# Performance work log

Hardware: AMD Instinct MI355X
Metric: run time of the kernel (lower is better)

Reference implementation:

```python
import jax, jax.numpy as jnp
import numpy as np

N_FFT = 1024
N_STAGES = 4
BASE = N_FFT >> N_STAGES          # 64: base-case DFT size
N_CHUNKS = 1 << N_STAGES          # 16 chunks after permutation
SPLIT0 = N_FFT // 2 + 1           # rfft output length (513)


def _mod_seq(order):
    mset = [0]
    for o in range(order):
        step = 2 ** o
        mset = [v for x in mset for v in (x, x + step)]
    return mset


def _perm_matrix(N, order):
    # faithful replica of get_fft_permutation_matrix
    m = np.zeros((N, N), dtype=np.float32)
    base = 2 ** order
    k = 0
    for p in _mod_seq(order):
        for j in range(N // base):
            m[j * base + p, k] = 1.0
            k += 1
    return m


def _twiddle(n):
    w = np.exp(-2j * np.pi / n) ** np.arange(n // 2)
    return (jnp.asarray(w.real.astype(np.float32)),
            jnp.asarray(w.imag.astype(np.float32)))


PERM = jnp.asarray(_perm_matrix(N_FFT, N_STAGES))
_dft = np.fft.fft(np.eye(BASE))
DFT_R = jnp.asarray(_dft.real.astype(np.float32))
DFT_I = jnp.asarray(_dft.imag.astype(np.float32))
# twiddle stage s combines blocks of size (N_FFT >> (N_STAGES - s)) into twice that
TWIDDLES = [_twiddle(N_FFT >> (N_STAGES - 1 - s)) for s in range(N_STAGES)]


def setup_inputs() -> dict:
    key = jax.random.key(0)
    x = jax.random.normal(key, (16, 512, N_FFT), dtype=jnp.float32)
    return {"x": x}


def reference(x):
    # 1) bit-reversal-style permutation, expressed (faithfully) as a matmul
    y = jnp.matmul(x, PERM)                                   # [B,T,N]
    blocks = y.reshape(*x.shape[:-1], N_CHUNKS, BASE)         # [B,T,C,base]
    blocks = jnp.moveaxis(blocks, -2, 0)                      # [C,B,T,base]
    # 2) base-case DFT via dense matmul (all dfts share the same matrix)
    br = jnp.matmul(blocks, DFT_R.T)
    bi = jnp.matmul(blocks, DFT_I.T)
    # 3) Cooley-Tukey twiddle stages; consecutive blocks pair as (even, odd)
    for wr, wi in TWIDDLES:
        er, orr = br[0::2], br[1::2]
        ei, oii = bi[0::2], bi[1::2]
        tr = wr * orr - wi * oii
        ti = wr * oii + wi * orr
        br = jnp.concatenate([er + tr, er - tr], axis=-1)
        bi = jnp.concatenate([ei + ti, ei - ti], axis=-1)
    real, imag = br[0], bi[0]                                 # [B,T,N]
    # 4) keep only the rfft half-spectrum
    return real[..., :SPLIT0], imag[..., :SPLIT0]
```

## Files before the change

### kernel.cpp

```cpp
#include <hip/hip_runtime.h>

#define N_FFT 1024
#define SPLIT0 513
#define PAD(a) ((a) + ((a) >> 5))

__global__ __launch_bounds__(256) void rfft1024_pairs(const float* __restrict__ x,
                                                      float* __restrict__ out,
                                                      int nrows) {
    __shared__ float bre[2][N_FFT + 32];
    __shared__ float bim[2][N_FFT + 32];

    const int t = threadIdx.x;
    const int pair = blockIdx.x;
    const float* __restrict__ r0 = x + (size_t)(2 * pair) * N_FFT;
    const float* __restrict__ r1 = r0 + N_FFT;

    #pragma unroll
    for (int c = 0; c < 4; ++c) {
        int i = t + 256 * c;
        bre[0][PAD(i)] = r0[i];
        bim[0][PAD(i)] = r1[i];
    }
    __syncthreads();

    const float CANG = -6.2831853071795864769f / 1024.0f;
    int src = 0;

    #pragma unroll
    for (int p = 0; p < 5; ++p) {
        const int m = 1 << (2 * p);
        const int k = t & (m - 1);
        const int jm = t - k;

        float ar = bre[src][PAD(t)],       ai = bim[src][PAD(t)];
        float br = bre[src][PAD(t + 256)], bi = bim[src][PAD(t + 256)];
        float cr = bre[src][PAD(t + 512)], ci = bim[src][PAD(t + 512)];
        float dr = bre[src][PAD(t + 768)], di = bim[src][PAD(t + 768)];

        float t0r = ar + cr, t0i = ai + ci;
        float t1r = ar - cr, t1i = ai - ci;
        float t2r = br + dr, t2i = bi + di;
        float t3r = br - dr, t3i = bi - di;

        float y0r = t0r + t2r, y0i = t0i + t2i;
        float y1r = t1r + t3i, y1i = t1i - t3r;
        float y2r = t0r - t2r, y2i = t0i - t2i;
        float y3r = t1r - t3i, y3i = t1i + t3r;

        float ang = CANG * (float)jm;
        float s1, c1;
        __sincosf(ang, &s1, &c1);
        float c2 = c1 * c1 - s1 * s1, s2 = 2.0f * c1 * s1;
        float c3 = c1 * c2 - s1 * s2, s3 = c1 * s2 + s1 * c2;

        float z1r = y1r * c1 - y1i * s1, z1i = y1r * s1 + y1i * c1;
        float z2r = y2r * c2 - y2i * s2, z2i = y2r * s2 + y2i * c2;
        float z3r = y3r * c3 - y3i * s3, z3i = y3r * s3 + y3i * c3;

        const int dst = src ^ 1;
        const int w0 = k + 4 * jm;
        bre[dst][PAD(w0)]          = y0r; bim[dst][PAD(w0)]          = y0i;
        bre[dst][PAD(w0 + m)]      = z1r; bim[dst][PAD(w0 + m)]      = z1i;
        bre[dst][PAD(w0 + 2 * m)]  = z2r; bim[dst][PAD(w0 + 2 * m)]  = z2i;
        bre[dst][PAD(w0 + 3 * m)]  = z3r; bim[dst][PAD(w0 + 3 * m)]  = z3i;
        __syncthreads();
        src ^= 1;
    }

    const size_t row0 = (size_t)(2 * pair);
    float* __restrict__ outr = out;
    float* __restrict__ outi = out + (size_t)nrows * SPLIT0;

    #pragma unroll
    for (int c = 0; c < 2; ++c) {
        int kk = t + 256 * c;
        float zr = bre[src][PAD(kk)], zi = bim[src][PAD(kk)];
        int km = (N_FFT - kk) & (N_FFT - 1);
        float mr = bre[src][PAD(km)], mi = bim[src][PAD(km)];
        float X0r = 0.5f * (zr + mr), X0i = 0.5f * (zi - mi);
        float X1r = 0.5f * (zi + mi), X1i = 0.5f * (mr - zr);
        outr[row0 * SPLIT0 + kk]       = X0r;
        outi[row0 * SPLIT0 + kk]       = X0i;
        outr[(row0 + 1) * SPLIT0 + kk] = X1r;
        outi[(row0 + 1) * SPLIT0 + kk] = X1i;
    }
    if (t == 0) {
        float zr = bre[src][PAD(512)], zi = bim[src][PAD(512)];
        outr[row0 * SPLIT0 + 512]       = zr;
        outi[row0 * SPLIT0 + 512]       = 0.0f;
        outr[(row0 + 1) * SPLIT0 + 512] = zi;
        outi[(row0 + 1) * SPLIT0 + 512] = 0.0f;
    }
}

extern "C" void kernel_launch(void* const* d_in, const int* in_sizes, int n_in,
                              void* d_out, int out_size, void* d_ws, size_t ws_size,
                              hipStream_t stream) {
    const float* x = (const float*)d_in[0];
    float* out = (float*)d_out;
    const int nrows = in_sizes[0] / N_FFT;
    rfft1024_pairs<<<nrows / 2, 256, 0, stream>>>(x, out, nrows);
}
```

Measured before the change: 83.11 us.

## Restructure FFT as single-wave radix-16 register passes with fewer LDS exchanges

Replaces the 256-thread kernel, which ran five radix-4 passes each with a shared-memory round trip, with one 64-lane wavefront per row pair. Each lane now holds 16 complex points in registers and does two radix-4 stages (a radix-16 step) per LDS exchange. Twiddles come from a single sincos per lane plus complex multiplies. The aim is to cut LDS traffic and block-wide barriers; the cost is much higher register pressure and less parallelism per block, which may lower occupancy.

```diff
diff --git a/kernel.cpp b/kernel.cpp
--- a/kernel.cpp
+++ b/kernel.cpp
@@ -4,91 +4,196 @@
 #define SPLIT0 513
 #define PAD(a) ((a) + ((a) >> 5))
 
-__global__ __launch_bounds__(256) void rfft1024_pairs(const float* __restrict__ x,
-                                                      float* __restrict__ out,
-                                                      int nrows) {
-    __shared__ float bre[2][N_FFT + 32];
-    __shared__ float bim[2][N_FFT + 32];
-
-    const int t = threadIdx.x;
+__device__ __forceinline__ void bfly4(
+    float ar, float ai, float br, float bi,
+    float cr, float ci, float dr, float di,
+    float w1r, float w1i, float w2r, float w2i, float w3r, float w3i,
+    float& y0r, float& y0i, float& y1r, float& y1i,
+    float& y2r, float& y2i, float& y3r, float& y3i)
+{
+    float t0r = ar + cr, t0i = ai + ci;
+    float t1r = ar - cr, t1i = ai - ci;
+    float t2r = br + dr, t2i = bi + di;
+    float t3r = br - dr, t3i = bi - di;
+    float u0r = t0r + t2r, u0i = t0i + t2i;
+    float u1r = t1r + t3i, u1i = t1i - t3r;
+    float u2r = t0r - t2r, u2i = t0i - t2i;
+    float u3r = t1r - t3i, u3i = t1i + t3r;
+    y0r = u0r;                 y0i = u0i;
+    y1r = u1r * w1r - u1i * w1i;  y1i = u1r * w1i + u1i * w1r;
+    y2r = u2r * w2r - u2i * w2i;  y2i = u2r * w2i + u2i * w2r;
+    y3r = u3r * w3r - u3i * w3i;  y3i = u3r * w3i + u3i * w3r;
+}
+
+__device__ __forceinline__ void cmul(float ar, float ai, float br, float bi,
+                                     float& cr, float& ci) {
+    cr = ar * br - ai * bi;
+    ci = ar * bi + ai * br;
+}
+
+__global__ __launch_bounds__(64) void rfft1024_wave(const float* __restrict__ x,
+                                                    float* __restrict__ out,
+                                                    int nrows) {
+    __shared__ float sre[1056];
+    __shared__ float sim[1056];
+
+    const int l = threadIdx.x;
     const int pair = blockIdx.x;
     const float* __restrict__ r0 = x + (size_t)(2 * pair) * N_FFT;
     const float* __restrict__ r1 = r0 + N_FFT;
 
-    #pragma unroll
-    for (int c = 0; c < 4; ++c) {
-        int i = t + 256 * c;
-        bre[0][PAD(i)] = r0[i];
-        bim[0][PAD(i)] = r1[i];
-    }
-    __syncthreads();
-
-    const float CANG = -6.2831853071795864769f / 1024.0f;
-    int src = 0;
-
-    #pragma unroll
-    for (int p = 0; p < 5; ++p) {
-        const int m = 1 << (2 * p);
-        const int k = t & (m - 1);
-        const int jm = t - k;
-
-        float ar = bre[src][PAD(t)],       ai = bim[src][PAD(t)];
-        float br = bre[src][PAD(t + 256)], bi = bim[src][PAD(t + 256)];
-        float cr = bre[src][PAD(t + 512)], ci = bim[src][PAD(t + 512)];
-        float dr = bre[src][PAD(t + 768)], di = bim[src][PAD(t + 768)];
-
+    float zr[16], zi[16];
+#pragma unroll
+    for (int w = 0; w < 16; ++w) {
+        zr[w] = r0[l + 64 * w];
+        zi[w] = r1[l + 64 * w];
+    }
+
+    const float C16R[4] = {1.0f, 0.92387953251128675613f,
+                           0.70710678118654752440f, 0.38268343236508977173f};
+    const float C16I[4] = {0.0f, -0.38268343236508977173f,
+                           -0.70710678118654752440f, -0.92387953251128675613f};
+    const float TWO_PI = 6.28318530717958647692f;
+
+    float wlr, wli;
+    { float s, c; __sincosf(-TWO_PI * (float)l * (1.0f / 1024.0f), &s, &c); wlr = c; wli = s; }
+
+    float o0r[4][4], o0i[4][4];
+#pragma unroll
+    for (int s = 0; s < 4; ++s) {
+        float w1r, w1i; cmul(wlr, wli, C16R[s], C16I[s], w1r, w1i);
+        float w2r, w2i; cmul(w1r, w1i, w1r, w1i, w2r, w2i);
+        float w3r, w3i; cmul(w1r, w1i, w2r, w2i, w3r, w3i);
+        bfly4(zr[s], zi[s], zr[s + 4], zi[s + 4], zr[s + 8], zi[s + 8], zr[s + 12], zi[s + 12],
+              w1r, w1i, w2r, w2i, w3r, w3i,
+              o0r[s][0], o0i[s][0], o0r[s][1], o0i[s][1],
+              o0r[s][2], o0i[s][2], o0r[s][3], o0i[s][3]);
+    }
+    float v1r[4][4], v1i[4][4];
+    {
+        float a2r, a2i; cmul(wlr, wli, wlr, wli, a2r, a2i);
+        float w1r, w1i; cmul(a2r, a2i, a2r, a2i, w1r, w1i);
+        float w2r, w2i; cmul(w1r, w1i, w1r, w1i, w2r, w2i);
+        float w3r, w3i; cmul(w1r, w1i, w2r, w2i, w3r, w3i);
+#pragma unroll
+        for (int p = 0; p < 4; ++p) {
+            bfly4(o0r[0][p], o0i[0][p], o0r[1][p], o0i[1][p],
+                  o0r[2][p], o0i[2][p], o0r[3][p], o0i[3][p],
+                  w1r, w1i, w2r, w2i, w3r, w3i,
+                  v1r[p][0], v1i[p][0], v1r[p][1], v1i[p][1],
+                  v1r[p][2], v1i[p][2], v1r[p][3], v1i[p][3]);
+        }
+    }
+
+#pragma unroll
+    for (int p = 0; p < 4; ++p)
+#pragma unroll
+        for (int r = 0; r < 4; ++r) {
+            int a = 16 * l + 4 * r + p;
+            sre[PAD(a)] = v1r[p][r];
+            sim[PAD(a)] = v1i[p][r];
+        }
+    __syncthreads();
+#pragma unroll
+    for (int w = 0; w < 16; ++w) {
+        int a = l + 64 * w;
+        zr[w] = sre[PAD(a)];
+        zi[w] = sim[PAD(a)];
+    }
+    __syncthreads();
+
+    const int k = l & 15, j0 = l >> 4;
+    float djr, dji;
+    { float s, c; __sincosf(-TWO_PI * (float)j0 * (1.0f / 64.0f), &s, &c); djr = c; dji = s; }
+
+    float o2r[4][4], o2i[4][4];
+#pragma unroll
+    for (int s = 0; s < 4; ++s) {
+        float w1r, w1i; cmul(djr, dji, C16R[s], C16I[s], w1r, w1i);
+        float w2r, w2i; cmul(w1r, w1i, w1r, w1i, w2r, w2i);
+        float w3r, w3i; cmul(w1r, w1i, w2r, w2i, w3r, w3i);
+        bfly4(zr[s], zi[s], zr[s + 4], zi[s + 4], zr[s + 8], zi[s + 8], zr[s + 12], zi[s + 12],
+              w1r, w1i, w2r, w2i, w3r, w3i,
+              o2r[s][0], o2i[s][0], o2r[s][1], o2i[s][1],
+              o2r[s][2], o2i[s][2], o2r[s][3], o2i[s][3]);
+    }
+    float v3r[4][4], v3i[4][4];
+    {
+        float b2r, b2i; cmul(djr, dji, djr, dji, b2r, b2i);
+        float e1r, e1i; cmul(b2r, b2i, b2r, b2i, e1r, e1i);
+        float e2r, e2i; cmul(e1r, e1i, e1r, e1i, e2r, e2i);
+        float e3r, e3i; cmul(e1r, e1i, e2r, e2i, e3r, e3i);
+#pragma unroll
+        for (int p = 0; p < 4; ++p) {
+            bfly4(o2r[0][p], o2i[0][p], o2r[1][p], o2i[1][p],
+                  o2r[2][p], o2i[2][p], o2r[3][p], o2i[3][p],
+                  e1r, e1i, e2r, e2i, e3r, e3i,
+                  v3r[p][0], v3i[p][0], v3r[p][1], v3i[p][1],
+                  v3r[p][2], v3i[p][2], v3r[p][3], v3i[p][3]);
+        }
+    }
+
+#pragma unroll
+    for (int p = 0; p < 4; ++p)
+#pragma unroll
+        for (int r = 0; r < 4; ++r) {
+            int a = 256 * j0 + 64 * r + 16 * p + k;
+            sre[PAD(a)] = v3r[p][r];
+            sim[PAD(a)] = v3i[p][r];
+        }
+    __syncthreads();
+#pragma unroll
+    for (int w = 0; w < 16; ++w) {
+        int a = l + 64 * w;
+        zr[w] = sre[PAD(a)];
+        zi[w] = sim[PAD(a)];
+    }
+    __syncthreads();
+
+#pragma unroll
+    for (int s = 0; s < 4; ++s) {
+        float ar = zr[s],      ai = zi[s];
+        float br = zr[s + 4],  bi = zi[s + 4];
+        float cr = zr[s + 8],  ci = zi[s + 8];
+        float dr = zr[s + 12], di = zi[s + 12];
         float t0r = ar + cr, t0i = ai + ci;
         float t1r = ar - cr, t1i = ai - ci;
         float t2r = br + dr, t2i = bi + di;
         float t3r = br - dr, t3i = bi - di;
-
         float y0r = t0r + t2r, y0i = t0i + t2i;
         float y1r = t1r + t3i, y1i = t1i - t3r;
         float y2r = t0r - t2r, y2i = t0i - t2i;
         float y3r = t1r - t3i, y3i = t1i + t3r;
-
-        float ang = CANG * (float)jm;
-        float s1, c1;
-        __sincosf(ang, &s1, &c1);
-        float c2 = c1 * c1 - s1 * s1, s2 = 2.0f * c1 * s1;
-        float c3 = c1 * c2 - s1 * s2, s3 = c1 * s2 + s1 * c2;
-
-        float z1r = y1r * c1 - y1i * s1, z1i = y1r * s1 + y1i * c1;
-        float z2r = y2r * c2 - y2i * s2, z2i = y2r * s2 + y2i * c2;
-        float z3r = y3r * c3 - y3i * s3, z3i = y3r * s3 + y3i * c3;
-
-        const int dst = src ^ 1;
-        const int w0 = k + 4 * jm;
-        bre[dst][PAD(w0)]          = y0r; bim[dst][PAD(w0)]          = y0i;
-        bre[dst][PAD(w0 + m)]      = z1r; bim[dst][PAD(w0 + m)]      = z1i;
-        bre[dst][PAD(w0 + 2 * m)]  = z2r; bim[dst][PAD(w0 + 2 * m)]  = z2i;
-        bre[dst][PAD(w0 + 3 * m)]  = z3r; bim[dst][PAD(w0 + 3 * m)]  = z3i;
-        __syncthreads();
-        src ^= 1;
-    }
+        int a0 = l + 64 * s;
+        sre[PAD(a0)]        = y0r;  sim[PAD(a0)]        = y0i;
+        sre[PAD(a0 + 256)]  = y1r;  sim[PAD(a0 + 256)]  = y1i;
+        sre[PAD(a0 + 512)]  = y2r;  sim[PAD(a0 + 512)]  = y2i;
+        sre[PAD(a0 + 768)]  = y3r;  sim[PAD(a0 + 768)]  = y3i;
+    }
+    __syncthreads();
 
     const size_t row0 = (size_t)(2 * pair);
     float* __restrict__ outr = out;
     float* __restrict__ outi = out + (size_t)nrows * SPLIT0;
 
-    #pragma unroll
-    for (int c = 0; c < 2; ++c) {
-        int kk = t + 256 * c;
-        float zr = bre[src][PAD(kk)], zi = bim[src][PAD(kk)];
+#pragma unroll
+    for (int w = 0; w < 8; ++w) {
+        int kk = l + 64 * w;
+        float a_r = sre[PAD(kk)], a_i = sim[PAD(kk)];
         int km = (N_FFT - kk) & (N_FFT - 1);
-        float mr = bre[src][PAD(km)], mi = bim[src][PAD(km)];
-        float X0r = 0.5f * (zr + mr), X0i = 0.5f * (zi - mi);
-        float X1r = 0.5f * (zi + mi), X1i = 0.5f * (mr - zr);
+        float m_r = sre[PAD(km)], m_i = sim[PAD(km)];
+        float X0r = 0.5f * (a_r + m_r), X0i = 0.5f * (a_i - m_i);
+        float X1r = 0.5f * (a_i + m_i), X1i = 0.5f * (m_r - a_r);
         outr[row0 * SPLIT0 + kk]       = X0r;
         outi[row0 * SPLIT0 + kk]       = X0i;
         outr[(row0 + 1) * SPLIT0 + kk] = X1r;
         outi[(row0 + 1) * SPLIT0 + kk] = X1i;
     }
-    if (t == 0) {
-        float zr = bre[src][PAD(512)], zi = bim[src][PAD(512)];
-        outr[row0 * SPLIT0 + 512]       = zr;
+    if (l == 0) {
+        float a_r = sre[PAD(512)], a_i = sim[PAD(512)];
+        outr[row0 * SPLIT0 + 512]       = a_r;
         outi[row0 * SPLIT0 + 512]       = 0.0f;
-        outr[(row0 + 1) * SPLIT0 + 512] = zi;
+        outr[(row0 + 1) * SPLIT0 + 512] = a_i;
         outi[(row0 + 1) * SPLIT0 + 512] = 0.0f;
     }
 }
@@ -99,5 +204,5 @@
     const float* x = (const float*)d_in[0];
     float* out = (float*)d_out;
     const int nrows = in_sizes[0] / N_FFT;
-    rfft1024_pairs<<<nrows / 2, 256, 0, stream>>>(x, out, nrows);
-}
+    rfft1024_wave<<<nrows / 2, 64, 0, stream>>>(x, out, nrows);
+}
```

Measured after the change: 83.25 us. About the same (+0.2%).
